# Kernel optimization log

Hardware: AMD Instinct MI355X
Metric: run time of the kernel (lower is better)

Reference implementation:

```python
import jax, jax.numpy as jnp
import numpy as np

DIM = 512
HEADS = 8
DIM_HEAD = 64  # scale constant from __init__; also dim // heads here
SCALE = DIM_HEAD ** -0.5


def setup_inputs() -> dict:
    key = jax.random.key(0)
    k1, k2, k3, k4 = jax.random.split(key, 4)
    x = jax.random.normal(k1, (2, 4096, DIM), dtype=jnp.float32)
    # nn.Linear weights: stored as [out, in]; we keep [in, out] for x @ W
    w_qkv = jax.random.normal(k2, (DIM, 3 * DIM), dtype=jnp.float32) * (DIM ** -0.5)
    w_out = jax.random.normal(k3, (DIM, DIM), dtype=jnp.float32) * (DIM ** -0.5)
    b_out = jax.random.normal(k4, (DIM,), dtype=jnp.float32) * 0.02
    return {"x": x, "w_qkv": w_qkv, "w_out": w_out, "b_out": b_out}


def reference(x, w_qkv, w_out, b_out):
    B, N, C = x.shape
    H = HEADS
    Dh = C // H
    qkv = x @ w_qkv                                   # [B, N, 3C]
    q, k, v = jnp.split(qkv, 3, axis=-1)
    # [B, N, C] -> [B, H, N, Dh]
    reshape = lambda t: t.reshape(B, N, H, Dh).transpose(0, 2, 1, 3)
    q, k, v = reshape(q), reshape(k), reshape(v)
    attn = jnp.einsum("bhnd,bhmd->bhnm", q, k) * SCALE  # [B, H, N, N]
    attn = jax.nn.softmax(attn, axis=-1)
    out = jnp.einsum("bhnm,bhmd->bhnd", attn, v)       # [B, H, N, Dh]
    out = out.transpose(0, 2, 1, 3).reshape(B, N, C)
    return out @ w_out + b_out
```

## Files before the change

kernel.cpp:

```cpp
#include <hip/hip_runtime.h>
#include <stdint.h>

typedef unsigned short u16;
typedef __bf16 bf16x8 __attribute__((ext_vector_type(8)));
typedef float fx4 __attribute__((ext_vector_type(4)));
typedef float fx16 __attribute__((ext_vector_type(16)));


__device__ __forceinline__ u16 f2bf(float f) {
    unsigned int u = __float_as_uint(f);
    u += 0x7fffu + ((u >> 16) & 1u);
    return (u16)(u >> 16);
}

__device__ __forceinline__ bf16x8 ld8(const u16* p) {
    return __builtin_bit_cast(bf16x8, *(const int4*)p);
}

__device__ __forceinline__ uint32_t pk2bf(float lo, float hi) {
    uint32_t a = __float_as_uint(lo) + 0x8000u;
    uint32_t b = __float_as_uint(hi) + 0x8000u;
    return __builtin_amdgcn_perm(b, a, 0x07060302u);
}


__global__ __launch_bounds__(256) void transpose_cast_kernel(const float* __restrict__ in,
                                                             u16* __restrict__ out,
                                                             int NR, int NC) {
    __shared__ float T[64][65];
    int t = threadIdx.x;
    int i0 = blockIdx.y * 64, j0 = blockIdx.x * 64;
    int r = t >> 4, cc = t & 15;
#pragma unroll
    for (int j = 0; j < 4; ++j) {
        int row = r + j * 16;
        float4 v = *(const float4*)(in + (size_t)(i0 + row) * NC + j0 + cc * 4);
        T[row][cc * 4 + 0] = v.x; T[row][cc * 4 + 1] = v.y;
        T[row][cc * 4 + 2] = v.z; T[row][cc * 4 + 3] = v.w;
    }
    __syncthreads();
#pragma unroll
    for (int j = 0; j < 4; ++j) {
        int jr = r + j * 16;
        unsigned int u0 = f2bf(T[cc * 4 + 0][jr]) | ((unsigned int)f2bf(T[cc * 4 + 1][jr]) << 16);
        unsigned int u1 = f2bf(T[cc * 4 + 2][jr]) | ((unsigned int)f2bf(T[cc * 4 + 3][jr]) << 16);
        uint2 u; u.x = u0; u.y = u1;
        *(uint2*)(out + (size_t)(j0 + jr) * NR + i0 + cc * 4) = u;
    }
}


#define QSCALE 0.180336880f

template<int MODE>
__global__ __launch_bounds__(256) void gemm_kernel(const void* __restrict__ Avoid,
                                                   const u16* __restrict__ Bt,
                                                   u16* __restrict__ Qf,
                                                   u16* __restrict__ Kf,
                                                   u16* __restrict__ Vf,
                                                   const float* __restrict__ bias,
                                                   float* __restrict__ Out,
                                                   int Ncols) {
    __shared__ __align__(16) u16 As[128 * 32];
    __shared__ __align__(16) u16 Bs[128 * 32];
    int tid = threadIdx.x;
    int w = tid >> 6, lane = tid & 63;
    int m16 = lane & 15, quad = lane >> 4;
    int ntn = Ncols / 128;
    int bx = blockIdx.x % ntn, by = blockIdx.x / ntn;
    int r0 = by * 128, c0 = bx * 128;
    int wr = w >> 1, wc = w & 1;

    fx4 acc[4][4] = {};

    for (int k0 = 0; k0 < 512; k0 += 32) {
        __syncthreads();
#pragma unroll
        for (int j = 0; j < 2; ++j) {
            int L = tid + j * 256;
            int row = L >> 2, c = L & 3;
            if (MODE == 0) {
                const float* af = (const float*)Avoid + (size_t)(r0 + row) * 512 + k0 + c * 8;
                float4 a = *(const float4*)af, b = *(const float4*)(af + 4);
                int4 v;
                v.x = (int)pk2bf(a.x, a.y); v.y = (int)pk2bf(a.z, a.w);
                v.z = (int)pk2bf(b.x, b.y); v.w = (int)pk2bf(b.z, b.w);
                *(int4*)&As[row * 32 + c * 8] = v;
            } else {
                const u16* ab = (const u16*)Avoid;
                *(int4*)&As[row * 32 + c * 8] = *(const int4*)(ab + (size_t)(r0 + row) * 512 + k0 + c * 8);
            }
            *(int4*)&Bs[row * 32 + c * 8] = *(const int4*)(Bt + (size_t)(c0 + row) * 512 + k0 + c * 8);
        }
        __syncthreads();
        bf16x8 af[4], bfr[4];
#pragma unroll
        for (int t = 0; t < 4; ++t) {
            af[t]  = ld8(&As[(wr * 64 + t * 16 + m16) * 32 + quad * 8]);
            bfr[t] = ld8(&Bs[(wc * 64 + t * 16 + m16) * 32 + quad * 8]);
        }
#pragma unroll
        for (int mt = 0; mt < 4; ++mt)
#pragma unroll
            for (int nt = 0; nt < 4; ++nt)
                acc[mt][nt] = __builtin_amdgcn_mfma_f32_16x16x32_bf16(af[mt], bfr[nt], acc[mt][nt], 0, 0, 0);
    }

#pragma unroll
    for (int mt = 0; mt < 4; ++mt) {
        int R0 = r0 + wr * 64 + mt * 16 + quad * 4;
#pragma unroll
        for (int nt = 0; nt < 4; ++nt) {
            int C = c0 + wc * 64 + nt * 16 + m16;
            if (MODE == 0) {
                int sec = C >> 9;
                int hd = (C >> 6) & 7, d = C & 63;
                int b = R0 >> 12, n0 = R0 & 4095;
                size_t hb = (size_t)(b * 8 + hd) * 262144;
                if (sec <= 1) {
                    u16* dst = (sec == 0) ? Qf : Kf;
                    float sc = (sec == 0) ? QSCALE : 1.0f;
                    size_t base = hb + (size_t)((n0 >> 5) * 4 + (d >> 4)) * 512
                                + ((d >> 3) & 1) * 256 + (n0 & 31) * 8 + (d & 7);
#pragma unroll
                    for (int r = 0; r < 4; ++r)
                        dst[base + r * 8] = f2bf(acc[mt][nt][r] * sc);
                } else {
                    size_t base = hb + (size_t)((n0 >> 6) * 8 + (d >> 5) * 4 + ((n0 >> 4) & 3)) * 512
                                + ((n0 >> 2) & 1) * 256 + (d & 31) * 8 + ((n0 >> 3) & 1) * 4;
                    unsigned int u0 = f2bf(acc[mt][nt][0]) | ((unsigned int)f2bf(acc[mt][nt][1]) << 16);
                    unsigned int u1 = f2bf(acc[mt][nt][2]) | ((unsigned int)f2bf(acc[mt][nt][3]) << 16);
                    uint2 u; u.x = u0; u.y = u1;
                    *(uint2*)(Vf + base) = u;
                }
            } else {
                float bv = bias[C];
#pragma unroll
                for (int r = 0; r < 4; ++r)
                    Out[(size_t)(R0 + r) * 512 + C] = acc[mt][nt][r] + bv;
            }
        }
    }
}


__device__ __forceinline__ void attn_iter(bf16x8 (&KC)[2][4], bf16x8 (&KN)[2][4],
                                          const bf16x8 (&qf)[4], const bf16x8& onesA,
                                          const fx16& Z,
                                          fx16& O0, fx16& O1, fx16& Lacc,
                                          const u16* __restrict__ Kh,
                                          const u16* __restrict__ Vh,
                                          int lane, int K0) {
    bf16x8 vf[2][4];
    {
        const u16* vb = Vh + (size_t)(K0 >> 6) * 4096 + lane * 8;
#pragma unroll
        for (int dt = 0; dt < 2; ++dt)
#pragma unroll
            for (int ch = 0; ch < 4; ++ch)
                vf[dt][ch] = ld8(vb + (dt * 4 + ch) * 512);
    }
    {
        int kn0 = (K0 + 64) & 4095;
        const u16* kb = Kh + (size_t)(kn0 >> 5) * 2048 + lane * 8;
#pragma unroll
        for (int dc = 0; dc < 4; ++dc) {
            KN[0][dc] = ld8(kb + dc * 512);
            KN[1][dc] = ld8(kb + 2048 + dc * 512);
        }
    }
    fx16 S0 = Z, S1 = Z;
#pragma unroll
    for (int dc = 0; dc < 4; ++dc) {
        S0 = __builtin_amdgcn_mfma_f32_32x32x16_bf16(KC[0][dc], qf[dc], S0, 0, 0, 0);
        S1 = __builtin_amdgcn_mfma_f32_32x32x16_bf16(KC[1][dc], qf[dc], S1, 0, 0, 0);
    }
    uint32_t pk0[8], pk1[8];
#pragma unroll
    for (int i = 0; i < 8; ++i) {
        pk0[i] = pk2bf(__builtin_amdgcn_exp2f(S0[2 * i]), __builtin_amdgcn_exp2f(S0[2 * i + 1]));
        pk1[i] = pk2bf(__builtin_amdgcn_exp2f(S1[2 * i]), __builtin_amdgcn_exp2f(S1[2 * i + 1]));
    }
#pragma unroll
    for (int c = 0; c < 4; ++c) {
        const uint32_t* pk = (c < 2) ? pk0 : pk1;
        int o = (c & 1) * 4;
        int4 bi; bi.x = (int)pk[o]; bi.y = (int)pk[o + 1]; bi.z = (int)pk[o + 2]; bi.w = (int)pk[o + 3];
        bf16x8 bfrag = __builtin_bit_cast(bf16x8, bi);
        O0 = __builtin_amdgcn_mfma_f32_32x32x16_bf16(vf[0][c], bfrag, O0, 0, 0, 0);
        O1 = __builtin_amdgcn_mfma_f32_32x32x16_bf16(vf[1][c], bfrag, O1, 0, 0, 0);
        Lacc = __builtin_amdgcn_mfma_f32_32x32x16_bf16(onesA, bfrag, Lacc, 0, 0, 0);
    }
}

__global__ __launch_bounds__(256, 2) void attn_kernel(const u16* __restrict__ Qf,
                                                      const u16* __restrict__ Kf,
                                                      const u16* __restrict__ Vf,
                                                      u16* __restrict__ Ob) {
    __shared__ __align__(16) u16 Eo[4 * 32 * 68];

    int tid = threadIdx.x;
    int w = tid >> 6, lane = tid & 63;
    int q32 = lane & 31, h = lane >> 5;
    int bh = ((blockIdx.x & 7) << 1) | ((blockIdx.x >> 3) & 1);
    int qt = blockIdx.x >> 4;
    int q0 = qt * 128;

    const u16* Qh = Qf + (size_t)bh * 262144;
    const u16* Kh = Kf + (size_t)bh * 262144;
    const u16* Vh = Vf + (size_t)bh * 262144;

    bf16x8 qf[4];
    {
        const u16* qb = Qh + (size_t)(qt * 4 + w) * 2048 + lane * 8;
#pragma unroll
        for (int dc = 0; dc < 4; ++dc)
            qf[dc] = ld8(qb + dc * 512);
    }

    int4 oi; oi.x = oi.y = oi.z = oi.w = 0x3F803F80;
    const bf16x8 onesA = __builtin_bit_cast(bf16x8, oi);
    const fx16 Z = {};
    fx16 O0 = {}, O1 = {}, Lacc = {};

    bf16x8 kA[2][4], kB[2][4];
    {
        const u16* kb = Kh + lane * 8;
#pragma unroll
        for (int dc = 0; dc < 4; ++dc) {
            kA[0][dc] = ld8(kb + dc * 512);
            kA[1][dc] = ld8(kb + 2048 + dc * 512);
        }
    }

    for (int k0 = 0; k0 < 4096; k0 += 128) {
        attn_iter(kA, kB, qf, onesA, Z, O0, O1, Lacc, Kh, Vh, lane, k0);
        attn_iter(kB, kA, qf, onesA, Z, O0, O1, Lacc, Kh, Vh, lane, k0 + 64);
    }

    float inv = 1.0f / Lacc[0];
    int ebase = w * 2176 + q32 * 68;
#pragma unroll
    for (int i = 0; i < 8; ++i) {
        int dbase = 8 * (i >> 1) + (i & 1) * 2 + 4 * h;
        uint32_t p0 = pk2bf(O0[2 * i] * inv, O0[2 * i + 1] * inv);
        uint32_t p1 = pk2bf(O1[2 * i] * inv, O1[2 * i + 1] * inv);
        *(uint32_t*)&Eo[ebase + dbase]      = p0;
        *(uint32_t*)&Eo[ebase + dbase + 32] = p1;
    }
    __syncthreads();
    int row = lane >> 1, half = lane & 1;
    int rb = w * 2176 + row * 68 + half * 32;
    int b = bh >> 3, hh = bh & 7;
    size_t gb = ((size_t)(b * 4096 + q0 + w * 32 + row)) * 512 + hh * 64 + half * 32;
#pragma unroll
    for (int s = 0; s < 4; ++s) {
        uint2 a = *(const uint2*)&Eo[rb + s * 8];
        uint2 c = *(const uint2*)&Eo[rb + s * 8 + 4];
        int4 v; v.x = (int)a.x; v.y = (int)a.y; v.z = (int)c.x; v.w = (int)c.y;
        *(int4*)(Ob + gb + s * 8) = v;
    }
}


extern "C" void kernel_launch(void* const* d_in, const int* in_sizes, int n_in,
                              void* d_out, int out_size, void* d_ws, size_t ws_size,
                              hipStream_t stream) {
    const float* x     = (const float*)d_in[0];
    const float* w_qkv = (const float*)d_in[1];
    const float* w_out = (const float*)d_in[2];
    const float* b_out = (const float*)d_in[3];
    float* out = (float*)d_out;

    char* ws = (char*)d_ws;
    u16* wqkv_t = (u16*)(ws);
    u16* wout_t = (u16*)(ws + 1572864);
    u16* Qfb    = (u16*)(ws + 2097152);
    u16* Kfb    = (u16*)(ws + 10485760);
    u16* Vfb    = (u16*)(ws + 18874368);
    u16* Ob     = (u16*)(ws + 27262976);

    transpose_cast_kernel<<<dim3(24, 8), 256, 0, stream>>>(w_qkv, wqkv_t, 512, 1536);
    transpose_cast_kernel<<<dim3(8, 8), 256, 0, stream>>>(w_out, wout_t, 512, 512);
    gemm_kernel<0><<<768, 256, 0, stream>>>(x, wqkv_t, Qfb, Kfb, Vfb, nullptr, nullptr, 1536);
    attn_kernel<<<512, 256, 0, stream>>>(Qfb, Kfb, Vfb, Ob);
    gemm_kernel<1><<<256, 256, 0, stream>>>(Ob, wout_t, nullptr, nullptr, nullptr, b_out, out, 512);
}
```

Before: 213.2 us.

## Split attention keys across two wave groups and use direct global-to-LDS loads in GEMM

```diff
diff --git a/kernel.cpp b/kernel.cpp
--- a/kernel.cpp
+++ b/kernel.cpp
@@ -21,6 +21,12 @@
     uint32_t a = __float_as_uint(lo) + 0x8000u;
     uint32_t b = __float_as_uint(hi) + 0x8000u;
     return __builtin_amdgcn_perm(b, a, 0x07060302u);
+}
+
+typedef __attribute__((address_space(3))) uint32_t lds_u32;
+typedef __attribute__((address_space(1))) const uint32_t glb_u32;
+__device__ __forceinline__ void glds16(const u16* g, u16* l) {
+    __builtin_amdgcn_global_load_lds((glb_u32*)g, (lds_u32*)l, 16, 0, 0);
 }
 
 
@@ -70,6 +76,7 @@
     int bx = blockIdx.x % ntn, by = blockIdx.x / ntn;
     int r0 = by * 128, c0 = bx * 128;
     int wr = w >> 1, wc = w & 1;
+    int lrow = lane >> 2, lchk = (lane & 3) * 8;
 
     fx4 acc[4][4] = {};
 
@@ -77,9 +84,10 @@
         __syncthreads();
 #pragma unroll
         for (int j = 0; j < 2; ++j) {
-            int L = tid + j * 256;
-            int row = L >> 2, c = L & 3;
+            int rw = j * 64 + w * 16;
             if (MODE == 0) {
+                int L = tid + j * 256;
+                int row = L >> 2, c = L & 3;
                 const float* af = (const float*)Avoid + (size_t)(r0 + row) * 512 + k0 + c * 8;
                 float4 a = *(const float4*)af, b = *(const float4*)(af + 4);
                 int4 v;
@@ -88,9 +96,9 @@
                 *(int4*)&As[row * 32 + c * 8] = v;
             } else {
                 const u16* ab = (const u16*)Avoid;
-                *(int4*)&As[row * 32 + c * 8] = *(const int4*)(ab + (size_t)(r0 + row) * 512 + k0 + c * 8);
+                glds16(ab + (size_t)(r0 + rw + lrow) * 512 + k0 + lchk, &As[rw * 32]);
             }
-            *(int4*)&Bs[row * 32 + c * 8] = *(const int4*)(Bt + (size_t)(c0 + row) * 512 + k0 + c * 8);
+            glds16(Bt + (size_t)(c0 + rw + lrow) * 512 + k0 + lchk, &Bs[rw * 32]);
         }
         __syncthreads();
         bf16x8 af[4], bfr[4];
@@ -161,7 +169,7 @@
                 vf[dt][ch] = ld8(vb + (dt * 4 + ch) * 512);
     }
     {
-        int kn0 = (K0 + 64) & 4095;
+        int kn0 = (K0 + 64) & 2047;
         const u16* kb = Kh + (size_t)(kn0 >> 5) * 2048 + lane * 8;
 #pragma unroll
         for (int dc = 0; dc < 4; ++dc) {
@@ -193,22 +201,24 @@
     }
 }
 
-__global__ __launch_bounds__(256, 2) void attn_kernel(const u16* __restrict__ Qf,
+__global__ __launch_bounds__(512, 4) void attn_kernel(const u16* __restrict__ Qf,
                                                       const u16* __restrict__ Kf,
                                                       const u16* __restrict__ Vf,
                                                       u16* __restrict__ Ob) {
     __shared__ __align__(16) u16 Eo[4 * 32 * 68];
+    __shared__ float Cmb[4][64][33];
 
     int tid = threadIdx.x;
-    int w = tid >> 6, lane = tid & 63;
+    int wave = tid >> 6, lane = tid & 63;
+    int w = wave & 3, half = wave >> 2;
     int q32 = lane & 31, h = lane >> 5;
     int bh = ((blockIdx.x & 7) << 1) | ((blockIdx.x >> 3) & 1);
     int qt = blockIdx.x >> 4;
     int q0 = qt * 128;
 
     const u16* Qh = Qf + (size_t)bh * 262144;
-    const u16* Kh = Kf + (size_t)bh * 262144;
-    const u16* Vh = Vf + (size_t)bh * 262144;
+    const u16* Kh = Kf + (size_t)bh * 262144 + (size_t)half * 131072;
+    const u16* Vh = Vf + (size_t)bh * 262144 + (size_t)half * 131072;
 
     bf16x8 qf[4];
     {
@@ -233,32 +243,45 @@
         }
     }
 
-    for (int k0 = 0; k0 < 4096; k0 += 128) {
+    for (int k0 = 0; k0 < 2048; k0 += 128) {
         attn_iter(kA, kB, qf, onesA, Z, O0, O1, Lacc, Kh, Vh, lane, k0);
         attn_iter(kB, kA, qf, onesA, Z, O0, O1, Lacc, Kh, Vh, lane, k0 + 64);
     }
 
-    float inv = 1.0f / Lacc[0];
-    int ebase = w * 2176 + q32 * 68;
-#pragma unroll
-    for (int i = 0; i < 8; ++i) {
-        int dbase = 8 * (i >> 1) + (i & 1) * 2 + 4 * h;
-        uint32_t p0 = pk2bf(O0[2 * i] * inv, O0[2 * i + 1] * inv);
-        uint32_t p1 = pk2bf(O1[2 * i] * inv, O1[2 * i + 1] * inv);
-        *(uint32_t*)&Eo[ebase + dbase]      = p0;
-        *(uint32_t*)&Eo[ebase + dbase + 32] = p1;
+    if (half == 1) {
+        float* dst = &Cmb[w][lane][0];
+#pragma unroll
+        for (int r = 0; r < 16; ++r) { dst[r] = O0[r]; dst[16 + r] = O1[r]; }
+        dst[32] = Lacc[0];
     }
     __syncthreads();
-    int row = lane >> 1, half = lane & 1;
-    int rb = w * 2176 + row * 68 + half * 32;
-    int b = bh >> 3, hh = bh & 7;
-    size_t gb = ((size_t)(b * 4096 + q0 + w * 32 + row)) * 512 + hh * 64 + half * 32;
-#pragma unroll
-    for (int s = 0; s < 4; ++s) {
-        uint2 a = *(const uint2*)&Eo[rb + s * 8];
-        uint2 c = *(const uint2*)&Eo[rb + s * 8 + 4];
-        int4 v; v.x = (int)a.x; v.y = (int)a.y; v.z = (int)c.x; v.w = (int)c.y;
-        *(int4*)(Ob + gb + s * 8) = v;
+    if (half == 0) {
+        const float* src = &Cmb[w][lane][0];
+#pragma unroll
+        for (int r = 0; r < 16; ++r) { O0[r] += src[r]; O1[r] += src[16 + r]; }
+        float inv = 1.0f / (Lacc[0] + src[32]);
+
+        int ebase = w * 2176 + q32 * 68;
+#pragma unroll
+        for (int i = 0; i < 8; ++i) {
+            int dbase = 8 * (i >> 1) + (i & 1) * 2 + 4 * h;
+            uint32_t p0 = pk2bf(O0[2 * i] * inv, O0[2 * i + 1] * inv);
+            uint32_t p1 = pk2bf(O1[2 * i] * inv, O1[2 * i + 1] * inv);
+            *(uint32_t*)&Eo[ebase + dbase]      = p0;
+            *(uint32_t*)&Eo[ebase + dbase + 32] = p1;
+        }
+        asm volatile("s_waitcnt lgkmcnt(0)" ::: "memory");
+        int row = lane >> 1, halfc = lane & 1;
+        int rb = w * 2176 + row * 68 + halfc * 32;
+        int b = bh >> 3, hh = bh & 7;
+        size_t gb = ((size_t)(b * 4096 + q0 + w * 32 + row)) * 512 + hh * 64 + halfc * 32;
+#pragma unroll
+        for (int s = 0; s < 4; ++s) {
+            uint2 a = *(const uint2*)&Eo[rb + s * 8];
+            uint2 c = *(const uint2*)&Eo[rb + s * 8 + 4];
+            int4 v; v.x = (int)a.x; v.y = (int)a.y; v.z = (int)c.x; v.w = (int)c.y;
+            *(int4*)(Ob + gb + s * 8) = v;
+        }
     }
 }
 
@@ -283,6 +306,6 @@
     transpose_cast_kernel<<<dim3(24, 8), 256, 0, stream>>>(w_qkv, wqkv_t, 512, 1536);
     transpose_cast_kernel<<<dim3(8, 8), 256, 0, stream>>>(w_out, wout_t, 512, 512);
     gemm_kernel<0><<<768, 256, 0, stream>>>(x, wqkv_t, Qfb, Kfb, Vfb, nullptr, nullptr, 1536);
-    attn_kernel<<<512, 256, 0, stream>>>(Qfb, Kfb, Vfb, Ob);
+    attn_kernel<<<512, 512, 0, stream>>>(Qfb, Kfb, Vfb, Ob);
     gemm_kernel<1><<<256, 256, 0, stream>>>(Ob, wout_t, nullptr, nullptr, nullptr, b_out, out, 512);
 }
```

Measured after the change: 343.4 us. 61.0% more time.
